# Kernel optimization log

Hardware: AMD Instinct MI355X
Metric: run time of the kernel (lower is better)

## Reference

```python
import jax, jax.numpy as jnp
import numpy as np

# Hardcoded skeleton graph from the source module (V=15 nodes, 28 directed edges)
_SRC = np.array([0,2,4,1,3,5,6,8,10,7,9,11,13,12,2,4,14,3,5,14,8,10,13,9,11,13,12,13])
_DST = np.array([2,4,14,3,5,14,8,10,13,9,11,13,14,13,0,2,4,1,3,5,6,8,10,7,9,11,13,14])
_V = 15

def _build_lhat():
    # PyG ChebConv norm with sym laplacian, lambda_max=2: L_hat = -D^{-1/2} A D^{-1/2}, diag 0
    A = np.zeros((_V, _V), np.float32)
    A[_DST, _SRC] = 1.0  # message flows src -> dst
    deg = A.sum(axis=1)
    dinv = np.where(deg > 0, deg ** -0.5, 0.0).astype(np.float32)
    return jnp.asarray(-(dinv[:, None] * A * dinv[None, :]))

_LHAT = _build_lhat()  # [V, V]

def _lstm_layer(xs, Wih, Whh, bih, bhh):
    # xs: [T, B, in]; torch LSTM gate order: i, f, g, o
    B = xs.shape[1]
    H = Whh.shape[1]
    b = bih + bhh
    def step(carry, xt):
        h, c = carry
        g = xt @ Wih.T + h @ Whh.T + b
        i, f, gg, o = jnp.split(g, 4, axis=-1)
        c = jax.nn.sigmoid(f) * c + jax.nn.sigmoid(i) * jnp.tanh(gg)
        h = jax.nn.sigmoid(o) * jnp.tanh(c)
        return (h, c), h
    init = (jnp.zeros((B, H), xs.dtype), jnp.zeros((B, H), xs.dtype))
    _, hs = jax.lax.scan(step, init, xs)
    return hs  # [T, B, H]

def setup_inputs() -> dict:
    key = jax.random.key(0)
    ks = jax.random.split(key, 16)
    N, C, T, V, M = 512, 3, 300, 15, 2
    H, IN, NC = 128, 45, 60
    s = 0.1
    return {
        "x1": jax.random.normal(ks[0], (N, C, T, V, M), jnp.float32),
        "x2": jax.random.normal(ks[1], (N, C, T, V, M), jnp.float32),
        "cheb_w0": jax.random.normal(ks[2], (3, 3), jnp.float32) * s,
        "cheb_w1": jax.random.normal(ks[3], (3, 3), jnp.float32) * s,
        "cheb_b": jax.random.normal(ks[4], (3,), jnp.float32) * s,
        "wih0": jax.random.normal(ks[5], (4 * H, IN), jnp.float32) * s,
        "whh0": jax.random.normal(ks[6], (4 * H, H), jnp.float32) * s,
        "bih0": jax.random.normal(ks[7], (4 * H,), jnp.float32) * s,
        "bhh0": jax.random.normal(ks[8], (4 * H,), jnp.float32) * s,
        "wih1": jax.random.normal(ks[9], (4 * H, H), jnp.float32) * s,
        "whh1": jax.random.normal(ks[10], (4 * H, H), jnp.float32) * s,
        "bih1": jax.random.normal(ks[11], (4 * H,), jnp.float32) * s,
        "bhh1": jax.random.normal(ks[12], (4 * H,), jnp.float32) * s,
        "fc_w": jax.random.normal(ks[13], (NC, H), jnp.float32) * np.sqrt(2.0 / NC).astype(np.float32),
        "fc_b": jax.random.normal(ks[14], (NC,), jnp.float32) * s,
    }

def reference(x1, x2, cheb_w0, cheb_w1, cheb_b, wih0, whh0, bih0, bhh0, wih1, whh1, bih1, bhh1, fc_w, fc_b):
    N, C, T, V, M = x1.shape
    # [N,C,T,V,M] -> [N*M*T, V, C]
    x = jnp.transpose(x1, (0, 4, 2, 3, 1)).reshape(N * M * T, V, C)
    # ChebConv K=2: out = Tx0 @ W0^T + Tx1 @ W1^T + b, Tx1 = L_hat @ x
    tx1 = jnp.einsum('ij,bjc->bic', _LHAT, x)
    x = x @ cheb_w0.T + tx1 @ cheb_w1.T + cheb_b
    # [N*M, T, V*C] -> time-major [T, N*M, V*C]
    seq = x.reshape(N * M, T, V * C).transpose(1, 0, 2)
    hs0 = _lstm_layer(seq, wih0, whh0, bih0, bhh0)
    hs1 = _lstm_layer(hs0, wih1, whh1, bih1, bhh1)
    h_last = hs1[-1]  # [N*M, 128]
    logits = h_last @ fc_w.T + fc_b
    return jax.nn.softmax(logits, axis=1)
```

## Files before the change

kernel.cpp:

```cpp
#include <hip/hip_runtime.h>
#include <hip/hip_fp16.h>

typedef _Float16 half_t;
typedef _Float16 half8 __attribute__((ext_vector_type(8)));
typedef float floatx4 __attribute__((ext_vector_type(4)));
typedef int   int4v  __attribute__((ext_vector_type(4)));

#define T_STEPS 300
#define NMB     1024
#define BS      16
#define NBLK    19

#define XT_OFF   0ULL
#define XT_BYTES ((unsigned long long)(T_STEPS*NMB + 16)*64*2)
#define HS0_OFF  (XT_OFF + XT_BYTES)
#define HS0_BYTES ((unsigned long long)(T_STEPS*NMB + 16)*128*2)
#define WCH_OFF  (HS0_OFF + HS0_BYTES)
#define WCH_BYTES (512ULL*64*2)
#define BC_OFF   (WCH_OFF + WCH_BYTES)
#define BC_BYTES (512ULL*4)
#define FLAG_OFF (BC_OFF + BC_BYTES)

#define S2 0.70710678118654752f
#define QH 0.5f
#define UU 0.40824829046386302f
#define TH 0.33333333333333333f
__constant__ float LHAT[225] = {
  0,0,-S2,0,0,0,0,0,0,0,0,0,0,0,0,
  0,0,0,-S2,0,0,0,0,0,0,0,0,0,0,0,
  -S2,0,0,0,-QH,0,0,0,0,0,0,0,0,0,0,
  0,-S2,0,0,0,-QH,0,0,0,0,0,0,0,0,0,
  0,0,-QH,0,0,0,0,0,0,0,0,0,0,0,-UU,
  0,0,0,-QH,0,0,0,0,0,0,0,0,0,0,-UU,
  0,0,0,0,0,0,0,0,-S2,0,0,0,0,0,0,
  0,0,0,0,0,0,0,0,0,-S2,0,0,0,0,0,
  0,0,0,0,0,0,-S2,0,0,0,-QH,0,0,0,0,
  0,0,0,0,0,0,0,-S2,0,0,0,-QH,0,0,0,
  0,0,0,0,0,0,0,0,-QH,0,0,0,0,-UU,0,
  0,0,0,0,0,0,0,0,0,-QH,0,0,0,-UU,0,
  0,0,0,0,0,0,0,0,0,0,0,0,0,0,0,
  0,0,0,0,0,0,0,0,0,0,-UU,-UU,0,0,0,
  0,0,0,0,-UU,-UU,0,0,0,0,0,0,0,-TH,0
};

__device__ __forceinline__ float frcp(float x)  { return __builtin_amdgcn_rcpf(x); }
__device__ __forceinline__ float fsig(float x)  { return frcp(1.f + __expf(-x)); }
__device__ __forceinline__ float ftanh(float x) { return 2.f*frcp(1.f + __expf(-2.f*x)) - 1.f; }

__device__ __forceinline__ half8 load_w8(const float* p) {
  const float4* q = (const float4*)p;
  float4 a = q[0], b = q[1];
  half8 f;
  f[0]=(half_t)a.x; f[1]=(half_t)a.y; f[2]=(half_t)a.z; f[3]=(half_t)a.w;
  f[4]=(half_t)b.x; f[5]=(half_t)b.y; f[6]=(half_t)b.z; f[7]=(half_t)b.w;
  return f;
}

__device__ __forceinline__ void pin(half8& f) {
  int4v t = __builtin_bit_cast(int4v, f);
  asm volatile("" : "+v"(t));
  f = __builtin_bit_cast(half8, t);
}
__device__ __forceinline__ void pinf(floatx4& f) {
  int4v t = __builtin_bit_cast(int4v, f);
  asm volatile("" : "+v"(t));
  f = __builtin_bit_cast(floatx4, t);
}

__device__ __forceinline__ void wait_flag(const int* f, int want, int tid) {
  if (tid == 0) {
    while (__hip_atomic_load(f, __ATOMIC_RELAXED, __HIP_MEMORY_SCOPE_AGENT) < want)
      __builtin_amdgcn_s_sleep(8);
    (void)__hip_atomic_load(f, __ATOMIC_ACQUIRE, __HIP_MEMORY_SCOPE_AGENT);
  }
  __syncthreads();
}

__global__ void k_prep(const float* __restrict__ w0, const float* __restrict__ w1,
                       const float* __restrict__ cb, const float* __restrict__ wih0,
                       const float* __restrict__ bih0, const float* __restrict__ bhh0,
                       half_t* __restrict__ wcomb_h, float* __restrict__ biasc,
                       int* __restrict__ flags) {
  const int n = threadIdx.x;
  if (n < 256) flags[n*16] = 0;
  float wrow[45];
  #pragma unroll
  for (int i=0;i<45;i++) wrow[i] = wih0[n*45+i];
  float P[45];
  #pragma unroll
  for (int i=0;i<15;i++)
    #pragma unroll
    for (int c=0;c<3;c++) {
      float s = 0.f;
      #pragma unroll
      for (int cp=0;cp<3;cp++) s += wrow[i*3+cp]*w1[cp*3+c];
      P[i*3+c] = s;
    }
  #pragma unroll
  for (int j=0;j<15;j++)
    #pragma unroll
    for (int c=0;c<3;c++) {
      float s = 0.f;
      #pragma unroll
      for (int cp=0;cp<3;cp++) s += wrow[j*3+cp]*w0[cp*3+c];
      #pragma unroll
      for (int i=0;i<15;i++) s += LHAT[i*15+j]*P[i*3+c];
      wcomb_h[n*64 + j*3+c] = (half_t)s;
    }
  for (int k=45;k<64;k++) wcomb_h[n*64+k] = (half_t)0.f;
  float b = bih0[n] + bhh0[n];
  #pragma unroll
  for (int i=0;i<15;i++)
    #pragma unroll
    for (int cp=0;cp<3;cp++) b += wrow[i*3+cp]*cb[cp];
  biasc[n] = b;
}

__launch_bounds__(512, 1)
__global__ void k_lstm_fused(const float* __restrict__ x1, const half_t* __restrict__ wch,
                             const float* __restrict__ biasc, const float* __restrict__ whh0,
                             half_t* __restrict__ hs0,
                             const float* __restrict__ wih1, const float* __restrict__ whh1,
                             const float* __restrict__ bih1, const float* __restrict__ bhh1,
                             const float* __restrict__ fcw, const float* __restrict__ fcb,
                             float* __restrict__ out, int* __restrict__ flags) {
  __shared__ __align__(16) char smem[80384];
  const int tid = threadIdx.x;
  const int wave = tid>>6, lane = tid&63, quad = lane>>4, l16 = lane&15;
  const bool qlo = quad < 2;
  const int brow = ((quad&1)<<2) | (quad&2);
  const int colw = wave*16 + l16;

  if (blockIdx.x < 128) {
    auto xs = (half_t (*)[BS][8][80])smem;
    auto hr = (half_t (*)[8][144])(smem + 40960);
    const int wg  = blockIdx.x;
    const int nm0 = wg*8;
    const int n0t3 = wg*4*3;
    int* flag = flags + wg*16;

    for (int i=tid; i<2*BS*8*80; i+=512) ((half_t*)smem)[i] = (half_t)0.f;
    for (int i=tid; i<8*144; i+=512) (&hr[15][0][0])[i] = (half_t)0.f;

    half8 whhF[4][4]; half8 wcF[4][2]; float bias[4];
    #pragma unroll
    for (int nt=0; nt<4; nt++) {
      const int gcol = nt*128 + colw;
      #pragma unroll
      for (int kc=0; kc<4; kc++) { whhF[nt][kc] = load_w8(whh0 + gcol*128 + kc*32 + quad*8); pin(whhF[nt][kc]); }
      #pragma unroll
      for (int kc=0; kc<2; kc++) { wcF[nt][kc] = *(const half8*)(wch + gcol*64 + kc*32 + quad*8); pin(wcF[nt][kc]); }
      bias[nt] = biasc[gcol];
    }
    float cst0 = 0.f, cst1 = 0.f;
    floatx4 z4 = {0.f,0.f,0.f,0.f}; pinf(z4);

    float2 xld[6];
    #define XDEC(IDX) const int v_=(IDX)%15; const int rA_=(IDX)/15; \
                      const int sh_=rA_&15; const int rB_=rA_>>4;    \
                      const int c_=rB_%3; const int nh_=rB_/3;
    #define XLOAD(TBASE) { _Pragma("unroll") for (int k=0;k<6;k++) { \
        const int idx=k*512+tid; if (idx<2880) { XDEC(idx)           \
          int tt=(TBASE)+sh_; if (tt>299) tt=299;                     \
          xld[k]=((const float2*)x1)[(size_t)((n0t3+nh_*3+c_)*300+tt)*15+v_]; } } }
    #define XWRITE(BUFI) { _Pragma("unroll") for (int k=0;k<6;k++) { \
        const int idx=k*512+tid; if (idx<2880) { XDEC(idx)           \
          xs[BUFI][sh_][nh_*2  ][v_*3+c_]=(half_t)xld[k].x;          \
          xs[BUFI][sh_][nh_*2+1][v_*3+c_]=(half_t)xld[k].y; } } }

    XLOAD(0); __syncthreads(); XWRITE(0);
    __syncthreads();

    for (int b=0; b<NBLK; b++) {
      const int bs = b*BS, buf = b&1;
      const int cnt = (T_STEPS - bs < BS) ? (T_STEPS - bs) : BS;
      const int ngr = cnt>>1;
      if (b+1 < NBLK) XLOAD(bs + BS);
      for (int g=0; g<ngr; g++) {
        const int s0 = g*2;
        floatx4 xp[4];
        {
          const half_t* xrow = &xs[buf][s0 + (l16>>3)][l16&7][0];
          #pragma unroll
          for (int nt=0; nt<4; nt++) xp[nt] = (floatx4){bias[nt],bias[nt],bias[nt],bias[nt]};
          #pragma unroll
          for (int kc=0; kc<2; kc++) {
            const half8 xa = *(const half8*)(xrow + kc*32 + quad*8);
            #pragma unroll
            for (int nt=0; nt<4; nt++)
              xp[nt] = __builtin_amdgcn_mfma_f32_16x16x32_f16(xa, wcF[nt][kc], xp[nt], 0,0,0);
          }
        }
        float xq0[4][2], xq2[4][2];
        #pragma unroll
        for (int nt=0; nt<4; nt++)
          #pragma unroll
          for (int r2=0; r2<2; r2++) {
            xq0[nt][r2] = __shfl_xor(xp[nt][r2],   32);
            xq2[nt][r2] = __shfl_xor(xp[nt][r2+2], 32);
          }
        #pragma unroll
        for (int js=0; js<2; js++) {
          const int t = bs + s0 + js;
          if (js==1 && g==0 && b+1 < NBLK) XWRITE(buf^1);
          floatx4 ah[4];
          #pragma unroll
          for (int nt=0; nt<4; nt++) ah[nt] = z4;
          {
            const half_t* hrow = &hr[(t+15)&15][l16&7][0];
            #pragma unroll
            for (int kc=0; kc<4; kc++) {
              const half8 ha = *(const half8*)(hrow + kc*32 + quad*8);
              #pragma unroll
              for (int nt=0; nt<4; nt++)
                ah[nt] = __builtin_amdgcn_mfma_f32_16x16x32_f16(ha, whhF[nt][kc], ah[nt], 0,0,0);
            }
          }
          #pragma unroll
          for (int r2=0; r2<2; r2++) {
            const float a0 = qlo ? ah[0][r2] : ah[0][r2+2];
            const float a1 = qlo ? ah[1][r2] : ah[1][r2+2];
            const float a2 = qlo ? ah[2][r2] : ah[2][r2+2];
            const float a3 = qlo ? ah[3][r2] : ah[3][r2+2];
            const float x0 = js==0 ? (qlo ? xp[0][r2] : xq2[0][r2]) : (qlo ? xq0[0][r2] : xp[0][r2+2]);
            const float x1v= js==0 ? (qlo ? xp[1][r2] : xq2[1][r2]) : (qlo ? xq0[1][r2] : xp[1][r2+2]);
            const float x2 = js==0 ? (qlo ? xp[2][r2] : xq2[2][r2]) : (qlo ? xq0[2][r2] : xp[2][r2+2]);
            const float x3 = js==0 ? (qlo ? xp[3][r2] : xq2[3][r2]) : (qlo ? xq0[3][r2] : xp[3][r2+2]);
            float& cst = r2 ? cst1 : cst0;
            cst = fsig(a1+x1v)*cst + fsig(a0+x0)*ftanh(a2+x2);
            hr[t&15][brow+r2][colw] = (half_t)(fsig(a3+x3)*ftanh(cst));
          }
          __syncthreads();
        }
      }
      {
        const int hS = tid>>5, hR = (tid>>2)&7, hC = (tid&3)*32;
        if (hS < cnt) {
          half_t* dst = hs0 + ((size_t)(bs+hS)*NMB + nm0 + hR)*128 + hC;
          #pragma unroll
          for (int k=0;k<4;k++) *(half8*)(dst + k*8) = *(const half8*)&hr[(bs+hS)&15][hR][hC + k*8];
        }
      }
      __syncthreads();
      if (tid == 0)
        __hip_atomic_store(flag, b+1, __ATOMIC_RELEASE, __HIP_MEMORY_SCOPE_AGENT);
    }
  } else {
    auto xs = (half_t (*)[BS][8][144])smem;
    auto h2 = (half_t (*)[8][144])(smem + 73728);
    float* logits_lds = (float*)(smem + 78336);
    const int wg  = blockIdx.x - 128;
    const int nm0 = wg*8;
    const int* flag = flags + wg*16;

    for (int i=tid; i<2*8*144; i+=512) (&h2[0][0][0])[i] = (half_t)0.f;

    half8 whF[4][4], wxF[4][4]; float bias[4];
    #pragma unroll
    for (int nt=0; nt<4; nt++) {
      const int gcol = nt*128 + colw;
      #pragma unroll
      for (int kc=0; kc<4; kc++) {
        wxF[nt][kc] = load_w8(wih1 + gcol*128 + kc*32 + quad*8); pin(wxF[nt][kc]);
        whF[nt][kc] = load_w8(whh1 + gcol*128 + kc*32 + quad*8); pin(whF[nt][kc]);
      }
      bias[nt] = bih1[gcol] + bhh1[gcol];
    }
    float cst0 = 0.f, cst1 = 0.f;
    floatx4 z4 = {0.f,0.f,0.f,0.f}; pinf(z4);

    const int sS = tid>>5, sR = (tid>>2)&7, sC = (tid&3)*32;
    float4 ld[4];
    wait_flag(flag, 1, tid);
    { const half_t* src = hs0 + ((size_t)sS*NMB + nm0 + sR)*128 + sC;
      #pragma unroll
      for (int k=0;k<4;k++) ld[k] = *(const float4*)(src + k*8); }
    #pragma unroll
    for (int k=0;k<4;k++) *(half8*)&xs[0][sS][sR][sC + k*8] = __builtin_bit_cast(half8, ld[k]);
    __syncthreads();

    for (int b=0; b<NBLK; b++) {
      const int bs = b*BS, buf = b&1;
      const int cnt = (T_STEPS - bs < BS) ? (T_STEPS - bs) : BS;
      const int ngr = cnt>>1;
      if (b+1 < NBLK) {
        wait_flag(flag, b+2, tid);
        int tt = bs + BS + sS; if (tt > 299) tt = 299;
        const half_t* src = hs0 + ((size_t)tt*NMB + nm0 + sR)*128 + sC;
        #pragma unroll
        for (int k=0;k<4;k++) ld[k] = *(const float4*)(src + k*8);
      }
      for (int g=0; g<ngr; g++) {
        const int s0 = g*2;
        floatx4 xp[4];
        {
          const half_t* xrow = &xs[buf][s0 + (l16>>3)][l16&7][0];
          #pragma unroll
          for (int nt=0; nt<4; nt++) xp[nt] = (floatx4){bias[nt],bias[nt],bias[nt],bias[nt]};
          #pragma unroll
          for (int kc=0; kc<4; kc++) {
            const half8 xa = *(const half8*)(xrow + kc*32 + quad*8);
            #pragma unroll
            for (int nt=0; nt<4; nt++)
              xp[nt] = __builtin_amdgcn_mfma_f32_16x16x32_f16(xa, wxF[nt][kc], xp[nt], 0,0,0);
          }
        }
        float xq0[4][2], xq2[4][2];
        #pragma unroll
        for (int nt=0; nt<4; nt++)
          #pragma unroll
          for (int r2=0; r2<2; r2++) {
            xq0[nt][r2] = __shfl_xor(xp[nt][r2],   32);
            xq2[nt][r2] = __shfl_xor(xp[nt][r2+2], 32);
          }
        #pragma unroll
        for (int js=0; js<2; js++) {
          const int t = bs + s0 + js;
          if (js==1 && g==0 && b+1 < NBLK) {
            #pragma unroll
            for (int k=0;k<4;k++) *(half8*)&xs[buf^1][sS][sR][sC + k*8] = __builtin_bit_cast(half8, ld[k]);
          }
          floatx4 ah[4];
          #pragma unroll
          for (int nt=0; nt<4; nt++) ah[nt] = z4;
          {
            const half_t* hrow = &h2[t&1][l16&7][0];
            #pragma unroll
            for (int kc=0; kc<4; kc++) {
              const half8 ha = *(const half8*)(hrow + kc*32 + quad*8);
              #pragma unroll
              for (int nt=0; nt<4; nt++)
                ah[nt] = __builtin_amdgcn_mfma_f32_16x16x32_f16(ha, whF[nt][kc], ah[nt], 0,0,0);
            }
          }
          #pragma unroll
          for (int r2=0; r2<2; r2++) {
            const float a0 = qlo ? ah[0][r2] : ah[0][r2+2];
            const float a1 = qlo ? ah[1][r2] : ah[1][r2+2];
            const float a2 = qlo ? ah[2][r2] : ah[2][r2+2];
            const float a3 = qlo ? ah[3][r2] : ah[3][r2+2];
            const float x0 = js==0 ? (qlo ? xp[0][r2] : xq2[0][r2]) : (qlo ? xq0[0][r2] : xp[0][r2+2]);
            const float x1v= js==0 ? (qlo ? xp[1][r2] : xq2[1][r2]) : (qlo ? xq0[1][r2] : xp[1][r2+2]);
            const float x2 = js==0 ? (qlo ? xp[2][r2] : xq2[2][r2]) : (qlo ? xq0[2][r2] : xp[2][r2+2]);
            const float x3 = js==0 ? (qlo ? xp[3][r2] : xq2[3][r2]) : (qlo ? xq0[3][r2] : xp[3][r2+2]);
            float& cst = r2 ? cst1 : cst0;
            cst = fsig(a1+x1v)*cst + fsig(a0+x0)*ftanh(a2+x2);
            h2[(t+1)&1][brow+r2][colw] = (half_t)(fsig(a3+x3)*ftanh(cst));
          }
          __syncthreads();
        }
      }
    }

    if (tid < 480) {
      const int rr = tid/60, cls = tid%60;
      float s = fcb[cls];
      for (int k2=0; k2<128; k2++) s += (float)h2[0][rr][k2] * fcw[cls*128+k2];
      logits_lds[rr*60+cls] = s;
    }
    __syncthreads();
    if (tid < 8) {
      float m = -1e30f;
      for (int j=0; j<60; j++) m = fmaxf(m, logits_lds[tid*60+j]);
      float s = 0.f;
      for (int j=0; j<60; j++) s += __expf(logits_lds[tid*60+j]-m);
      const float inv = frcp(s);
      for (int j=0; j<60; j++) out[(nm0+tid)*60+j] = __expf(logits_lds[tid*60+j]-m)*inv;
    }
  }
}

extern "C" void kernel_launch(void* const* d_in, const int* in_sizes, int n_in,
                              void* d_out, int out_size, void* d_ws, size_t ws_size,
                              hipStream_t stream) {
  const float* x1      = (const float*)d_in[0];
  const float* cheb_w0 = (const float*)d_in[2];
  const float* cheb_w1 = (const float*)d_in[3];
  const float* cheb_b  = (const float*)d_in[4];
  const float* wih0    = (const float*)d_in[5];
  const float* whh0    = (const float*)d_in[6];
  const float* bih0    = (const float*)d_in[7];
  const float* bhh0    = (const float*)d_in[8];
  const float* wih1    = (const float*)d_in[9];
  const float* whh1    = (const float*)d_in[10];
  const float* bih1    = (const float*)d_in[11];
  const float* bhh1    = (const float*)d_in[12];
  const float* fc_w    = (const float*)d_in[13];
  const float* fc_b    = (const float*)d_in[14];

  char* ws = (char*)d_ws;
  half_t* hs0   = (half_t*)(ws + HS0_OFF);
  half_t* wch   = (half_t*)(ws + WCH_OFF);
  float*  biasc = (float*)(ws + BC_OFF);
  int*    flags = (int*)(ws + FLAG_OFF);

  k_prep<<<dim3(1), dim3(512), 0, stream>>>(cheb_w0, cheb_w1, cheb_b, wih0, bih0, bhh0, wch, biasc, flags);
  k_lstm_fused<<<dim3(256), dim3(512), 0, stream>>>(
      x1, wch, biasc, whh0, hs0, wih1, whh1, bih1, bhh1, fc_w, fc_b, (float*)d_out, flags);
}
```

Before: 458.3 us.

## Remap MFMA A-row layout so each lane owns its gate outputs without shuffles

```diff
diff --git a/kernel.cpp b/kernel.cpp
--- a/kernel.cpp
+++ b/kernel.cpp
@@ -10,6 +10,9 @@
 #define NMB     1024
 #define BS      16
 #define NBLK    19
+
+#define XP0 88
+#define HP  152
 
 #define XT_OFF   0ULL
 #define XT_BYTES ((unsigned long long)(T_STEPS*NMB + 16)*64*2)
@@ -124,23 +127,21 @@
                              const float* __restrict__ bih1, const float* __restrict__ bhh1,
                              const float* __restrict__ fcw, const float* __restrict__ fcb,
                              float* __restrict__ out, int* __restrict__ flags) {
-  __shared__ __align__(16) char smem[80384];
+  __shared__ __align__(16) char smem[84640];
   const int tid = threadIdx.x;
   const int wave = tid>>6, lane = tid&63, quad = lane>>4, l16 = lane&15;
-  const bool qlo = quad < 2;
-  const int brow = ((quad&1)<<2) | (quad&2);
   const int colw = wave*16 + l16;
 
   if (blockIdx.x < 128) {
-    auto xs = (half_t (*)[BS][8][80])smem;
-    auto hr = (half_t (*)[8][144])(smem + 40960);
+    auto xs = (half_t (*)[BS][8][XP0])smem;
+    auto hr = (half_t (*)[8][HP])(smem + 45056);
     const int wg  = blockIdx.x;
     const int nm0 = wg*8;
     const int n0t3 = wg*4*3;
     int* flag = flags + wg*16;
 
-    for (int i=tid; i<2*BS*8*80; i+=512) ((half_t*)smem)[i] = (half_t)0.f;
-    for (int i=tid; i<8*144; i+=512) (&hr[15][0][0])[i] = (half_t)0.f;
+    for (int i=tid; i<2*BS*8*XP0; i+=512) ((half_t*)smem)[i] = (half_t)0.f;
+    for (int i=tid; i<8*HP; i+=512) (&hr[15][0][0])[i] = (half_t)0.f;
 
     half8 whhF[4][4]; half8 wcF[4][2]; float bias[4];
     #pragma unroll
@@ -156,16 +157,16 @@
     floatx4 z4 = {0.f,0.f,0.f,0.f}; pinf(z4);
 
     float2 xld[6];
-    #define XDEC(IDX) const int v_=(IDX)%15; const int rA_=(IDX)/15; \
-                      const int sh_=rA_&15; const int rB_=rA_>>4;    \
-                      const int c_=rB_%3; const int nh_=rB_/3;
-    #define XLOAD(TBASE) { _Pragma("unroll") for (int k=0;k<6;k++) { \
-        const int idx=k*512+tid; if (idx<2880) { XDEC(idx)           \
-          int tt=(TBASE)+sh_; if (tt>299) tt=299;                     \
-          xld[k]=((const float2*)x1)[(size_t)((n0t3+nh_*3+c_)*300+tt)*15+v_]; } } }
-    #define XWRITE(BUFI) { _Pragma("unroll") for (int k=0;k<6;k++) { \
-        const int idx=k*512+tid; if (idx<2880) { XDEC(idx)           \
-          xs[BUFI][sh_][nh_*2  ][v_*3+c_]=(half_t)xld[k].x;          \
+    #define XLOAD(TBASE) { _Pragma("unroll") for (int k=0;k<6;k++) {          \
+        const int idx=k*512+tid; const int v_=idx&15;                          \
+        if (v_<15) { const int sh_=(idx>>4)&15; const int rB_=idx>>8;          \
+          int tt=(TBASE)+sh_; if (tt>299) tt=299;                              \
+          xld[k]=((const float2*)x1)[(size_t)((n0t3+rB_)*300+tt)*15+v_]; } } }
+    #define XWRITE(BUFI) { _Pragma("unroll") for (int k=0;k<6;k++) {          \
+        const int idx=k*512+tid; const int v_=idx&15;                          \
+        if (v_<15) { const int sh_=(idx>>4)&15; const int rB_=idx>>8;          \
+          const int nh_=rB_/3, c_=rB_-3*(rB_/3);                               \
+          xs[BUFI][sh_][nh_*2  ][v_*3+c_]=(half_t)xld[k].x;                    \
           xs[BUFI][sh_][nh_*2+1][v_*3+c_]=(half_t)xld[k].y; } } }
 
     XLOAD(0); __syncthreads(); XWRITE(0);
@@ -180,7 +181,7 @@
         const int s0 = g*2;
         floatx4 xp[4];
         {
-          const half_t* xrow = &xs[buf][s0 + (l16>>3)][l16&7][0];
+          const half_t* xrow = &xs[buf][s0 + (l16&1)][l16>>1][0];
           #pragma unroll
           for (int nt=0; nt<4; nt++) xp[nt] = (floatx4){bias[nt],bias[nt],bias[nt],bias[nt]};
           #pragma unroll
@@ -191,14 +192,6 @@
               xp[nt] = __builtin_amdgcn_mfma_f32_16x16x32_f16(xa, wcF[nt][kc], xp[nt], 0,0,0);
           }
         }
-        float xq0[4][2], xq2[4][2];
-        #pragma unroll
-        for (int nt=0; nt<4; nt++)
-          #pragma unroll
-          for (int r2=0; r2<2; r2++) {
-            xq0[nt][r2] = __shfl_xor(xp[nt][r2],   32);
-            xq2[nt][r2] = __shfl_xor(xp[nt][r2+2], 32);
-          }
         #pragma unroll
         for (int js=0; js<2; js++) {
           const int t = bs + s0 + js;
@@ -207,7 +200,7 @@
           #pragma unroll
           for (int nt=0; nt<4; nt++) ah[nt] = z4;
           {
-            const half_t* hrow = &hr[(t+15)&15][l16&7][0];
+            const half_t* hrow = &hr[(t+15)&15][l16>>1][0];
             #pragma unroll
             for (int kc=0; kc<4; kc++) {
               const half8 ha = *(const half8*)(hrow + kc*32 + quad*8);
@@ -217,18 +210,15 @@
             }
           }
           #pragma unroll
-          for (int r2=0; r2<2; r2++) {
-            const float a0 = qlo ? ah[0][r2] : ah[0][r2+2];
-            const float a1 = qlo ? ah[1][r2] : ah[1][r2+2];
-            const float a2 = qlo ? ah[2][r2] : ah[2][r2+2];
-            const float a3 = qlo ? ah[3][r2] : ah[3][r2+2];
-            const float x0 = js==0 ? (qlo ? xp[0][r2] : xq2[0][r2]) : (qlo ? xq0[0][r2] : xp[0][r2+2]);
-            const float x1v= js==0 ? (qlo ? xp[1][r2] : xq2[1][r2]) : (qlo ? xq0[1][r2] : xp[1][r2+2]);
-            const float x2 = js==0 ? (qlo ? xp[2][r2] : xq2[2][r2]) : (qlo ? xq0[2][r2] : xp[2][r2+2]);
-            const float x3 = js==0 ? (qlo ? xp[3][r2] : xq2[3][r2]) : (qlo ? xq0[3][r2] : xp[3][r2+2]);
-            float& cst = r2 ? cst1 : cst0;
-            cst = fsig(a1+x1v)*cst + fsig(a0+x0)*ftanh(a2+x2);
-            hr[t&15][brow+r2][colw] = (half_t)(fsig(a3+x3)*ftanh(cst));
+          for (int bb=0; bb<2; bb++) {
+            const int r = bb*2 + js;
+            const float gi = ah[0][r] + xp[0][r];
+            const float gf = ah[1][r] + xp[1][r];
+            const float gg = ah[2][r] + xp[2][r];
+            const float go = ah[3][r] + xp[3][r];
+            float& cst = bb ? cst1 : cst0;
+            cst = fsig(gf)*cst + fsig(gi)*ftanh(gg);
+            hr[t&15][quad*2+bb][colw] = (half_t)(fsig(go)*ftanh(cst));
           }
           __syncthreads();
         }
@@ -246,14 +236,14 @@
         __hip_atomic_store(flag, b+1, __ATOMIC_RELEASE, __HIP_MEMORY_SCOPE_AGENT);
     }
   } else {
-    auto xs = (half_t (*)[BS][8][144])smem;
-    auto h2 = (half_t (*)[8][144])(smem + 73728);
-    float* logits_lds = (float*)(smem + 78336);
+    auto xs = (half_t (*)[BS][8][HP])smem;
+    auto h2 = (half_t (*)[8][HP])(smem + 77824);
+    float* logits_lds = (float*)(smem + 82688);
     const int wg  = blockIdx.x - 128;
     const int nm0 = wg*8;
     const int* flag = flags + wg*16;
 
-    for (int i=tid; i<2*8*144; i+=512) (&h2[0][0][0])[i] = (half_t)0.f;
+    for (int i=tid; i<2*8*HP; i+=512) (&h2[0][0][0])[i] = (half_t)0.f;
 
     half8 whF[4][4], wxF[4][4]; float bias[4];
     #pragma unroll
@@ -294,7 +284,7 @@
         const int s0 = g*2;
         floatx4 xp[4];
         {
-          const half_t* xrow = &xs[buf][s0 + (l16>>3)][l16&7][0];
+          const half_t* xrow = &xs[buf][s0 + (l16&1)][l16>>1][0];
           #pragma unroll
           for (int nt=0; nt<4; nt++) xp[nt] = (floatx4){bias[nt],bias[nt],bias[nt],bias[nt]};
           #pragma unroll
@@ -305,14 +295,6 @@
               xp[nt] = __builtin_amdgcn_mfma_f32_16x16x32_f16(xa, wxF[nt][kc], xp[nt], 0,0,0);
           }
         }
-        float xq0[4][2], xq2[4][2];
-        #pragma unroll
-        for (int nt=0; nt<4; nt++)
-          #pragma unroll
-          for (int r2=0; r2<2; r2++) {
-            xq0[nt][r2] = __shfl_xor(xp[nt][r2],   32);
-            xq2[nt][r2] = __shfl_xor(xp[nt][r2+2], 32);
-          }
         #pragma unroll
         for (int js=0; js<2; js++) {
           const int t = bs + s0 + js;
@@ -324,7 +306,7 @@
           #pragma unroll
           for (int nt=0; nt<4; nt++) ah[nt] = z4;
           {
-            const half_t* hrow = &h2[t&1][l16&7][0];
+            const half_t* hrow = &h2[t&1][l16>>1][0];
             #pragma unroll
             for (int kc=0; kc<4; kc++) {
               const half8 ha = *(const half8*)(hrow + kc*32 + quad*8);
@@ -334,18 +316,15 @@
             }
           }
           #pragma unroll
-          for (int r2=0; r2<2; r2++) {
-            const float a0 = qlo ? ah[0][r2] : ah[0][r2+2];
-            const float a1 = qlo ? ah[1][r2] : ah[1][r2+2];
-            const float a2 = qlo ? ah[2][r2] : ah[2][r2+2];
-            const float a3 = qlo ? ah[3][r2] : ah[3][r2+2];
-            const float x0 = js==0 ? (qlo ? xp[0][r2] : xq2[0][r2]) : (qlo ? xq0[0][r2] : xp[0][r2+2]);
-            const float x1v= js==0 ? (qlo ? xp[1][r2] : xq2[1][r2]) : (qlo ? xq0[1][r2] : xp[1][r2+2]);
-            const float x2 = js==0 ? (qlo ? xp[2][r2] : xq2[2][r2]) : (qlo ? xq0[2][r2] : xp[2][r2+2]);
-            const float x3 = js==0 ? (qlo ? xp[3][r2] : xq2[3][r2]) : (qlo ? xq0[3][r2] : xp[3][r2+2]);
-            float& cst = r2 ? cst1 : cst0;
-            cst = fsig(a1+x1v)*cst + fsig(a0+x0)*ftanh(a2+x2);
-            h2[(t+1)&1][brow+r2][colw] = (half_t)(fsig(a3+x3)*ftanh(cst));
+          for (int bb=0; bb<2; bb++) {
+            const int r = bb*2 + js;
+            const float gi = ah[0][r] + xp[0][r];
+            const float gf = ah[1][r] + xp[1][r];
+            const float gg = ah[2][r] + xp[2][r];
+            const float go = ah[3][r] + xp[3][r];
+            float& cst = bb ? cst1 : cst0;
+            cst = fsig(gf)*cst + fsig(gi)*ftanh(gg);
+            h2[(t+1)&1][quad*2+bb][colw] = (half_t)(fsig(go)*ftanh(cst));
           }
           __syncthreads();
         }
```

New measurement: 430.3 us. 1.06x faster.
